# Performance work log

Hardware: AMD Instinct MI355X
Metric: run time of the kernel (lower is better)

## Reference

```python
import jax, jax.numpy as jnp
import numpy as np
from jax import lax

S, V, E, H, T = 2048, 50257, 512, 1024, 12
HD = H // 2  # per-direction hidden
START, END = 0, 1
NEG = -1e6


def setup_inputs() -> dict:
    key = jax.random.key(0)
    ks = jax.random.split(key, 16)
    sentence = jax.random.randint(ks[0], (S,), 0, V)
    gold_tags = jax.random.randint(ks[1], (S,), 2, T)  # avoid START/END gold labels
    emb = jax.random.normal(ks[2], (V, E), jnp.float32) * 0.1
    s = 0.05
    wih_f = jax.random.normal(ks[3], (4 * HD, E), jnp.float32) * s
    whh_f = jax.random.normal(ks[4], (4 * HD, HD), jnp.float32) * s
    b_f = jax.random.normal(ks[5], (4 * HD,), jnp.float32) * s
    wih_b = jax.random.normal(ks[6], (4 * HD, E), jnp.float32) * s
    whh_b = jax.random.normal(ks[7], (4 * HD, HD), jnp.float32) * s
    b_b = jax.random.normal(ks[8], (4 * HD,), jnp.float32) * s
    w_out = jax.random.normal(ks[9], (T, H), jnp.float32) * s
    b_out = jax.random.normal(ks[10], (T,), jnp.float32) * s
    transitions = jax.random.normal(ks[11], (T, T), jnp.float32)
    transitions = transitions.at[START, :].set(NEG).at[:, END].set(NEG)
    h0 = jax.random.normal(ks[12], (2, HD), jnp.float32)
    c0 = jax.random.normal(ks[13], (2, HD), jnp.float32)
    return dict(sentence=sentence, gold_tags=gold_tags, emb=emb,
                wih_f=wih_f, whh_f=whh_f, b_f=b_f,
                wih_b=wih_b, whh_b=whh_b, b_b=b_b,
                w_out=w_out, b_out=b_out, transitions=transitions,
                h0=h0, c0=c0)


def _lstm_dir(x, h0, c0, wih, whh, b):
    # x: [S, E] -> hidden states [S, HD]; PyTorch gate order i,f,g,o
    def step(carry, xt):
        h, c = carry
        g = xt @ wih.T + h @ whh.T + b
        i, f, gg, o = jnp.split(g, 4)
        i, f, o = jax.nn.sigmoid(i), jax.nn.sigmoid(f), jax.nn.sigmoid(o)
        c = f * c + i * jnp.tanh(gg)
        h = o * jnp.tanh(c)
        return (h, c), h
    _, hs = lax.scan(step, (h0, c0), x)
    return hs


def _feats(sentence, emb, wih_f, whh_f, b_f, wih_b, whh_b, b_b, w_out, b_out, h0, c0):
    x = emb[sentence]                                  # [S, E]
    hf = _lstm_dir(x, h0[0], c0[0], wih_f, whh_f, b_f)  # [S, HD]
    hb = _lstm_dir(x[::-1], h0[1], c0[1], wih_b, whh_b, b_b)[::-1]
    return jnp.concatenate([hf, hb], axis=1) @ w_out.T + b_out  # [S, T]


def _crf_nll(feats, gold_tags, transitions):
    # forward algorithm (log partition)
    init = jnp.full((T,), NEG, feats.dtype).at[START].set(0.0)
    def step(prev, feat):
        nxt = jax.nn.logsumexp(prev[None, :] + transitions + feat[:, None], axis=1)
        return nxt, None
    final, _ = lax.scan(step, init, feats)
    alpha = jax.nn.logsumexp(final + transitions[END])
    # gold score
    tags = jnp.concatenate([jnp.array([START], gold_tags.dtype), gold_tags])
    trans_score = jnp.sum(transitions[tags[1:], tags[:-1]])
    emit_score = jnp.sum(feats[jnp.arange(feats.shape[0]), tags[1:]])
    gold = trans_score + emit_score + transitions[END, tags[-1]]
    return alpha - gold


def reference(sentence, gold_tags, emb, wih_f, whh_f, b_f, wih_b, whh_b, b_b,
              w_out, b_out, transitions, h0, c0):
    feats = _feats(sentence, emb, wih_f, whh_f, b_f, wih_b, whh_b, b_b,
                   w_out, b_out, h0, c0)
    return _crf_nll(feats, gold_tags, transitions)
```

## Files before the change

### kernel.cpp

```cpp
#include <hip/hip_runtime.h>
#include <hip/hip_bf16.h>

#define S 2048
#define HD 512
#define EDIM 512
#define NT 12
#define G4 2048
#define NWGD 64
#define RPW 32
#define JPW 8
#define HSTR 36

typedef unsigned short ushort_t;
typedef unsigned int uint_t;

__device__ __forceinline__ ushort_t f2b(float f) {
    uint_t u = __float_as_uint(f);
    uint_t r = u + 0x7fffu + ((u >> 16) & 1u);
    return (ushort_t)(r >> 16);
}
__device__ __forceinline__ float b2f(ushort_t h) {
    return __uint_as_float(((uint_t)h) << 16);
}
__device__ __forceinline__ float sigm(float x) { return 1.f / (1.f + __expf(-x)); }
__device__ __forceinline__ float tanh_(float x) {
    float e = __expf(2.f * x);
    return 1.f - 2.f / (e + 1.f);
}

__global__ __launch_bounds__(256, 2)
void xw_gemm(const int* __restrict__ sentence, const float* __restrict__ emb,
             const float* __restrict__ wih_f, const float* __restrict__ b_f,
             const float* __restrict__ wih_b, const float* __restrict__ b_b,
             ushort_t* __restrict__ xw) {
    __shared__ float As[32][68];
    __shared__ float Bs[32][68];
    __shared__ int toks[64];
    const int tid = threadIdx.x;
    const int tbase = blockIdx.x * 64;
    const int rbase = blockIdx.y * 64;
    const int dir = blockIdx.z;
    const float* wih = dir ? wih_b : wih_f;
    const float* bia = dir ? b_b : b_f;
    if (tid < 64) {
        int tt = tbase + tid;
        toks[tid] = sentence[dir ? (S - 1 - tt) : tt];
    }
    __syncthreads();
    const int lm = tid >> 2;
    const int lk = (tid & 3) * 8;
    const int ty = tid >> 4, tx = tid & 15;
    const float* aBase = emb + (size_t)toks[lm] * EDIM + lk;
    const float* bBase = wih + (size_t)(rbase + lm) * EDIM + lk;
    float acc[4][4];
#pragma unroll
    for (int i = 0; i < 4; ++i)
#pragma unroll
        for (int j = 0; j < 4; ++j) acc[i][j] = 0.f;

    for (int kc = 0; kc < EDIM; kc += 32) {
        float4 a0 = ((const float4*)(aBase + kc))[0];
        float4 a1 = ((const float4*)(aBase + kc))[1];
        float4 b0 = ((const float4*)(bBase + kc))[0];
        float4 b1 = ((const float4*)(bBase + kc))[1];
        __syncthreads();
        As[lk + 0][lm] = a0.x; As[lk + 1][lm] = a0.y; As[lk + 2][lm] = a0.z; As[lk + 3][lm] = a0.w;
        As[lk + 4][lm] = a1.x; As[lk + 5][lm] = a1.y; As[lk + 6][lm] = a1.z; As[lk + 7][lm] = a1.w;
        Bs[lk + 0][lm] = b0.x; Bs[lk + 1][lm] = b0.y; Bs[lk + 2][lm] = b0.z; Bs[lk + 3][lm] = b0.w;
        Bs[lk + 4][lm] = b1.x; Bs[lk + 5][lm] = b1.y; Bs[lk + 6][lm] = b1.z; Bs[lk + 7][lm] = b1.w;
        __syncthreads();
#pragma unroll
        for (int kk = 0; kk < 32; ++kk) {
            float4 a4 = *(const float4*)&As[kk][ty * 4];
            float4 b4 = *(const float4*)&Bs[kk][tx * 4];
            float av[4] = {a4.x, a4.y, a4.z, a4.w};
            float bv[4] = {b4.x, b4.y, b4.z, b4.w};
#pragma unroll
            for (int i = 0; i < 4; ++i)
#pragma unroll
                for (int j = 0; j < 4; ++j) acc[i][j] = fmaf(av[i], bv[j], acc[i][j]);
        }
    }
    float4 bi = *(const float4*)&bia[rbase + tx * 4];
    float bvv[4] = {bi.x, bi.y, bi.z, bi.w};
#pragma unroll
    for (int i = 0; i < 4; ++i) {
        ushort4 o;
        o.x = f2b(acc[i][0] + bvv[0]);
        o.y = f2b(acc[i][1] + bvv[1]);
        o.z = f2b(acc[i][2] + bvv[2]);
        o.w = f2b(acc[i][3] + bvv[3]);
        ushort_t* p = xw + ((size_t)dir * S + tbase + ty * 4 + i) * G4 + rbase + tx * 4;
        *(ushort4*)p = o;
    }
}

__global__ __launch_bounds__(256, 1)
void lstm_rec(const float* __restrict__ whh_f, const float* __restrict__ whh_b,
              const float* __restrict__ h0, const float* __restrict__ c0,
              const ushort_t* __restrict__ xw, float* hs) {
    __shared__ float hstage[16 * HSTR];
    __shared__ float gates[RPW];
    const int tid = threadIdx.x;
    const int dir = blockIdx.x >> 6;
    const int wg = blockIdx.x & 63;
    const int jbase = wg * JPW;
    const int rg = tid >> 4, kc = tid & 15;
    const float* whh = dir ? whh_b : whh_f;

    int grow[2];
#pragma unroll
    for (int ri = 0; ri < 2; ++ri) {
        int r = rg * 2 + ri;
        grow[ri] = (r >> 3) * HD + jbase + (r & 7);
    }
    float4 w[2][8];
#pragma unroll
    for (int ri = 0; ri < 2; ++ri)
#pragma unroll
        for (int i = 0; i < 8; ++i)
            w[ri][i] = *(const float4*)&whh[(size_t)grow[ri] * HD + kc * 32 + i * 4];

    const ushort_t* xwd = xw + (size_t)dir * S * G4;
    float* hsd = hs + (size_t)dir * S * HD;

    float cj = 0.f;
    if (tid < JPW) cj = c0[dir * HD + jbase + tid];

    {
        int c = tid >> 4, m = (2 * tid) & 31;
        hstage[c * HSTR + m] = h0[dir * HD + 2 * tid];
        hstage[c * HSTR + m + 1] = h0[dir * HD + 2 * tid + 1];
    }
    __syncthreads();

    const bool isw = (kc == 0);
    for (int t = 0; t < S; ++t) {
        float xv0 = 0.f, xv1 = 0.f;
        if (isw) {
            xv0 = b2f(xwd[(size_t)t * G4 + grow[0]]);
            xv1 = b2f(xwd[(size_t)t * G4 + grow[1]]);
        }
        float a0 = 0.f, a1 = 0.f;
#pragma unroll
        for (int i = 0; i < 8; ++i) {
            float4 h4 = *(const float4*)&hstage[kc * HSTR + i * 4];
            a0 = fmaf(w[0][i].x, h4.x, a0); a0 = fmaf(w[0][i].y, h4.y, a0);
            a0 = fmaf(w[0][i].z, h4.z, a0); a0 = fmaf(w[0][i].w, h4.w, a0);
            a1 = fmaf(w[1][i].x, h4.x, a1); a1 = fmaf(w[1][i].y, h4.y, a1);
            a1 = fmaf(w[1][i].z, h4.z, a1); a1 = fmaf(w[1][i].w, h4.w, a1);
        }
#pragma unroll
        for (int m = 1; m < 16; m <<= 1) {
            a0 += __shfl_xor(a0, m);
            a1 += __shfl_xor(a1, m);
        }
        if (isw) {
            gates[rg * 2] = a0 + xv0;
            gates[rg * 2 + 1] = a1 + xv1;
        }
        __syncthreads();
        if (tid < JPW) {
            float ai = gates[tid], af = gates[JPW + tid];
            float ag = gates[2 * JPW + tid], ao = gates[3 * JPW + tid];
            float ii = sigm(ai), ff = sigm(af), gg = tanh_(ag), oo = sigm(ao);
            cj = ff * cj + ii * gg;
            float hnew = oo * tanh_(cj);
            __hip_atomic_store(&hsd[(size_t)t * HD + jbase + tid], hnew,
                               __ATOMIC_RELAXED, __HIP_MEMORY_SCOPE_AGENT);
        }
        if (t < S - 1) {
            const unsigned long long* p0 =
                (const unsigned long long*)&hsd[(size_t)t * HD + 2 * tid];
            float v0, v1;
            for (;;) {
                unsigned long long v =
                    __hip_atomic_load(p0, __ATOMIC_RELAXED, __HIP_MEMORY_SCOPE_AGENT);
                uint_t lo = (uint_t)v, hi = (uint_t)(v >> 32);
                if (lo != 0xFFFFFFFFu && hi != 0xFFFFFFFFu) {
                    v0 = __uint_as_float(lo);
                    v1 = __uint_as_float(hi);
                    break;
                }
            }
            int c = tid >> 4, m = (2 * tid) & 31;
            hstage[c * HSTR + m] = v0;
            hstage[c * HSTR + m + 1] = v1;
        }
        __syncthreads();
    }
}

__global__ __launch_bounds__(256)
void feats_k(const float* __restrict__ hs, const float* __restrict__ w_out,
             const float* __restrict__ b_out, float* __restrict__ feats) {
    const int t = blockIdx.x, tid = threadIdx.x;
    float4 h4;
    if (tid < 128)
        h4 = *(const float4*)&hs[(size_t)t * HD + tid * 4];
    else
        h4 = *(const float4*)&hs[(size_t)S * HD + (size_t)(S - 1 - t) * HD + (tid - 128) * 4];
    float acc[NT];
#pragma unroll
    for (int tg = 0; tg < NT; ++tg) {
        float4 w4 = *(const float4*)&w_out[(size_t)tg * 1024 + tid * 4];
        acc[tg] = h4.x * w4.x + h4.y * w4.y + h4.z * w4.z + h4.w * w4.w;
    }
#pragma unroll
    for (int m = 1; m < 64; m <<= 1)
#pragma unroll
        for (int tg = 0; tg < NT; ++tg) acc[tg] += __shfl_xor(acc[tg], m);
    __shared__ float part[4][NT];
    if ((tid & 63) == 0) {
#pragma unroll
        for (int tg = 0; tg < NT; ++tg) part[tid >> 6][tg] = acc[tg];
    }
    __syncthreads();
    if (tid < NT)
        feats[(size_t)t * NT + tid] =
            part[0][tid] + part[1][tid] + part[2][tid] + part[3][tid] + b_out[tid];
}

__global__ __launch_bounds__(256, 1)
void crf_k(const float* __restrict__ feats, const int* __restrict__ gold,
           const float* __restrict__ trans, float* __restrict__ out) {
    extern __shared__ float sfeats[];
    __shared__ float red[256];
    __shared__ float nprev[NT];
    __shared__ float tr[144];
    __shared__ float gold_sh;
    const int tid = threadIdx.x;
    for (int i = tid; i < S * NT / 4; i += 256)
        ((float4*)sfeats)[i] = ((const float4*)feats)[i];
    if (tid < 144) tr[tid] = trans[tid];
    __syncthreads();
    float gsum = 0.f;
    for (int t = tid; t < S; t += 256) {
        int a = gold[t];
        int b = t ? gold[t - 1] : 0;
        gsum += tr[a * NT + b] + sfeats[t * NT + a];
    }
    red[tid] = gsum;
    __syncthreads();
    for (int s = 128; s; s >>= 1) {
        if (tid < s) red[tid] += red[tid + s];
        __syncthreads();
    }
    if (tid == 0) gold_sh = red[0] + tr[1 * NT + gold[S - 1]];
    __syncthreads();
    const int i = tid >> 4, j = tid & 15;
    const bool act = (tid < 192) && (j < NT);
    float tij = act ? tr[i * NT + j] : -3e38f;
    float prev = (j == 0) ? 0.f : -1e6f;
    for (int t = 0; t < S; ++t) {
        float v = act ? (prev + tij) : -3e38f;
        float mx = v;
        mx = fmaxf(mx, __shfl_xor(mx, 1));
        mx = fmaxf(mx, __shfl_xor(mx, 2));
        mx = fmaxf(mx, __shfl_xor(mx, 4));
        mx = fmaxf(mx, __shfl_xor(mx, 8));
        float e = __expf(v - mx);
        float ss = e;
        ss += __shfl_xor(ss, 1);
        ss += __shfl_xor(ss, 2);
        ss += __shfl_xor(ss, 4);
        ss += __shfl_xor(ss, 8);
        if (tid < 192 && j == 0) nprev[i] = mx + __logf(ss) + sfeats[t * NT + i];
        __syncthreads();
        prev = nprev[j < NT ? j : 0];
        __syncthreads();
    }
    if (tid < 64) {
        float v2 = (tid < NT) ? prev + tr[1 * NT + tid] : -3e38f;
        float mx = v2;
        mx = fmaxf(mx, __shfl_xor(mx, 1));
        mx = fmaxf(mx, __shfl_xor(mx, 2));
        mx = fmaxf(mx, __shfl_xor(mx, 4));
        mx = fmaxf(mx, __shfl_xor(mx, 8));
        float e = __expf(v2 - mx);
        float ss = e;
        ss += __shfl_xor(ss, 1);
        ss += __shfl_xor(ss, 2);
        ss += __shfl_xor(ss, 4);
        ss += __shfl_xor(ss, 8);
        if (tid == 0) out[0] = (mx + __logf(ss)) - gold_sh;
    }
}

extern "C" void kernel_launch(void* const* d_in, const int* in_sizes, int n_in,
                              void* d_out, int out_size, void* d_ws, size_t ws_size,
                              hipStream_t stream) {
    const int* sentence = (const int*)d_in[0];
    const int* gold = (const int*)d_in[1];
    const float* emb = (const float*)d_in[2];
    const float* wih_f = (const float*)d_in[3];
    const float* whh_f = (const float*)d_in[4];
    const float* b_f = (const float*)d_in[5];
    const float* wih_b = (const float*)d_in[6];
    const float* whh_b = (const float*)d_in[7];
    const float* b_b = (const float*)d_in[8];
    const float* w_out = (const float*)d_in[9];
    const float* b_out = (const float*)d_in[10];
    const float* trans = (const float*)d_in[11];
    const float* h0 = (const float*)d_in[12];
    const float* c0 = (const float*)d_in[13];
    float* out = (float*)d_out;

    char* ws = (char*)d_ws;
    const size_t XW_B = (size_t)2 * S * G4 * 2;
    const size_t HS_B = (size_t)2 * S * HD * 4;
    ushort_t* xw = (ushort_t*)ws;
    float* hs = (float*)(ws + XW_B);
    float* feats = (float*)(ws + XW_B + HS_B);

    hipMemsetAsync(hs, 0xFF, HS_B, stream);

    dim3 gg(S / 64, G4 / 64, 2);
    xw_gemm<<<gg, 256, 0, stream>>>(sentence, emb, wih_f, b_f, wih_b, b_b, xw);

    lstm_rec<<<2 * NWGD, 256, 0, stream>>>(whh_f, whh_b, h0, c0, xw, hs);

    feats_k<<<S, 256, 0, stream>>>(hs, w_out, b_out, feats);

    const size_t CRF_LDS = (size_t)S * NT * 4;
    hipFuncSetAttribute((const void*)crf_k,
                        hipFuncAttributeMaxDynamicSharedMemorySize, (int)CRF_LDS);
    crf_k<<<1, 256, CRF_LDS, stream>>>(feats, gold, trans, out);
}
```

Before: 5.393 ms.

## Make LSTM recurrence wave-independent with per-wave h copies and staged transposed xw

The input projection output is written transposed (gate-row major, time contiguous) so each wave can prefetch 64 timesteps of its gate inputs into LDS in a double buffer. Within the recurrent kernel, each wave now owns two hidden units: it computes all four gate dot products using 8 lanes per row, reduces with shuffles, and keeps a private copy of the full hidden state in LDS. This removes both __syncthreads per timestep and the shared gates buffer. Each wave polls global memory for the full previous h vector, which raises global polling traffic per step, and correctness now depends on per-wave program order.

Measured after the change: 8.596 ms. 1.59x slower.

```diff
diff --git a/kernel.cpp b/kernel.cpp
--- a/kernel.cpp
+++ b/kernel.cpp
@@ -7,9 +7,7 @@
 #define NT 12
 #define G4 2048
 #define NWGD 64
-#define RPW 32
 #define JPW 8
-#define HSTR 36
 
 typedef unsigned short ushort_t;
 typedef unsigned int uint_t;
@@ -32,7 +30,7 @@
 void xw_gemm(const int* __restrict__ sentence, const float* __restrict__ emb,
              const float* __restrict__ wih_f, const float* __restrict__ b_f,
              const float* __restrict__ wih_b, const float* __restrict__ b_b,
-             ushort_t* __restrict__ xw) {
+             ushort_t* __restrict__ xwT) {
     __shared__ float As[32][68];
     __shared__ float Bs[32][68];
     __shared__ int toks[64];
@@ -58,11 +56,11 @@
 #pragma unroll
         for (int j = 0; j < 4; ++j) acc[i][j] = 0.f;
 
-    for (int kc = 0; kc < EDIM; kc += 32) {
-        float4 a0 = ((const float4*)(aBase + kc))[0];
-        float4 a1 = ((const float4*)(aBase + kc))[1];
-        float4 b0 = ((const float4*)(bBase + kc))[0];
-        float4 b1 = ((const float4*)(bBase + kc))[1];
+    for (int kcc = 0; kcc < EDIM; kcc += 32) {
+        float4 a0 = ((const float4*)(aBase + kcc))[0];
+        float4 a1 = ((const float4*)(aBase + kcc))[1];
+        float4 b0 = ((const float4*)(bBase + kcc))[0];
+        float4 b1 = ((const float4*)(bBase + kcc))[1];
         __syncthreads();
         As[lk + 0][lm] = a0.x; As[lk + 1][lm] = a0.y; As[lk + 2][lm] = a0.z; As[lk + 3][lm] = a0.w;
         As[lk + 4][lm] = a1.x; As[lk + 5][lm] = a1.y; As[lk + 6][lm] = a1.z; As[lk + 7][lm] = a1.w;
@@ -84,13 +82,13 @@
     float4 bi = *(const float4*)&bia[rbase + tx * 4];
     float bvv[4] = {bi.x, bi.y, bi.z, bi.w};
 #pragma unroll
-    for (int i = 0; i < 4; ++i) {
+    for (int j = 0; j < 4; ++j) {
         ushort4 o;
-        o.x = f2b(acc[i][0] + bvv[0]);
-        o.y = f2b(acc[i][1] + bvv[1]);
-        o.z = f2b(acc[i][2] + bvv[2]);
-        o.w = f2b(acc[i][3] + bvv[3]);
-        ushort_t* p = xw + ((size_t)dir * S + tbase + ty * 4 + i) * G4 + rbase + tx * 4;
+        o.x = f2b(acc[0][j] + bvv[j]);
+        o.y = f2b(acc[1][j] + bvv[j]);
+        o.z = f2b(acc[2][j] + bvv[j]);
+        o.w = f2b(acc[3][j] + bvv[j]);
+        ushort_t* p = xwT + ((size_t)dir * G4 + rbase + tx * 4 + j) * S + tbase + ty * 4;
         *(ushort4*)p = o;
     }
 }
@@ -98,96 +96,106 @@
 __global__ __launch_bounds__(256, 1)
 void lstm_rec(const float* __restrict__ whh_f, const float* __restrict__ whh_b,
               const float* __restrict__ h0, const float* __restrict__ c0,
-              const ushort_t* __restrict__ xw, float* hs) {
-    __shared__ float hstage[16 * HSTR];
-    __shared__ float gates[RPW];
+              const ushort_t* __restrict__ xwT, float* hs) {
+    __shared__ float hstage[4 * 544];
+    __shared__ ushort_t xstage[4][2][512];
     const int tid = threadIdx.x;
+    const int wv = tid >> 6;
+    const int lw = tid & 63;
     const int dir = blockIdx.x >> 6;
     const int wg = blockIdx.x & 63;
     const int jbase = wg * JPW;
-    const int rg = tid >> 4, kc = tid & 15;
+    const int kc = lw & 7;
+    const int gate = (lw >> 3) & 3;
+    const int jl = lw >> 5;
+    const int jglob = jbase + wv * 2 + jl;
+    const int row = gate * HD + jglob;
     const float* whh = dir ? whh_b : whh_f;
 
-    int grow[2];
-#pragma unroll
-    for (int ri = 0; ri < 2; ++ri) {
-        int r = rg * 2 + ri;
-        grow[ri] = (r >> 3) * HD + jbase + (r & 7);
-    }
-    float4 w[2][8];
-#pragma unroll
-    for (int ri = 0; ri < 2; ++ri)
-#pragma unroll
-        for (int i = 0; i < 8; ++i)
-            w[ri][i] = *(const float4*)&whh[(size_t)grow[ri] * HD + kc * 32 + i * 4];
-
-    const ushort_t* xwd = xw + (size_t)dir * S * G4;
+    float4 w[16];
+#pragma unroll
+    for (int i = 0; i < 16; ++i)
+        w[i] = *(const float4*)&whh[(size_t)row * HD + kc * 64 + i * 4];
+
+    const ushort_t* xwd = xwT + (size_t)dir * G4 * S;
     float* hsd = hs + (size_t)dir * S * HD;
 
-    float cj = 0.f;
-    if (tid < JPW) cj = c0[dir * HD + jbase + tid];
-
+    const int ri = lw >> 3;
+    const ushort_t* sbase = xwd + (size_t)((ri >> 1) * HD + jbase + wv * 2 + (ri & 1)) * S;
     {
-        int c = tid >> 4, m = (2 * tid) & 31;
-        hstage[c * HSTR + m] = h0[dir * HD + 2 * tid];
-        hstage[c * HSTR + m + 1] = h0[dir * HD + 2 * tid + 1];
-    }
-    __syncthreads();
-
-    const bool isw = (kc == 0);
+        uint4 vch = *(const uint4*)(sbase + (lw & 7) * 8);
+        *(uint4*)&xstage[wv][0][ri * 64 + (lw & 7) * 8] = vch;
+    }
+
+    const bool upd = (lw & 31) == 0;
+    float cj = upd ? c0[dir * HD + jglob] : 0.f;
+
+    {
+        float4 a = *(const float4*)&h0[dir * HD + lw * 8];
+        float4 b4 = *(const float4*)&h0[dir * HD + lw * 8 + 4];
+        float* d = &hstage[wv * 544 + (lw >> 3) * 68 + (lw & 7) * 8];
+        *(float4*)d = a;
+        *(float4*)(d + 4) = b4;
+    }
+
+    const float* hb = &hstage[wv * 544 + kc * 68];
     for (int t = 0; t < S; ++t) {
-        float xv0 = 0.f, xv1 = 0.f;
-        if (isw) {
-            xv0 = b2f(xwd[(size_t)t * G4 + grow[0]]);
-            xv1 = b2f(xwd[(size_t)t * G4 + grow[1]]);
-        }
-        float a0 = 0.f, a1 = 0.f;
-#pragma unroll
-        for (int i = 0; i < 8; ++i) {
-            float4 h4 = *(const float4*)&hstage[kc * HSTR + i * 4];
-            a0 = fmaf(w[0][i].x, h4.x, a0); a0 = fmaf(w[0][i].y, h4.y, a0);
-            a0 = fmaf(w[0][i].z, h4.z, a0); a0 = fmaf(w[0][i].w, h4.w, a0);
-            a1 = fmaf(w[1][i].x, h4.x, a1); a1 = fmaf(w[1][i].y, h4.y, a1);
-            a1 = fmaf(w[1][i].z, h4.z, a1); a1 = fmaf(w[1][i].w, h4.w, a1);
-        }
-#pragma unroll
-        for (int m = 1; m < 16; m <<= 1) {
-            a0 += __shfl_xor(a0, m);
-            a1 += __shfl_xor(a1, m);
-        }
-        if (isw) {
-            gates[rg * 2] = a0 + xv0;
-            gates[rg * 2 + 1] = a1 + xv1;
-        }
-        __syncthreads();
-        if (tid < JPW) {
-            float ai = gates[tid], af = gates[JPW + tid];
-            float ag = gates[2 * JPW + tid], ao = gates[3 * JPW + tid];
-            float ii = sigm(ai), ff = sigm(af), gg = tanh_(ag), oo = sigm(ao);
-            cj = ff * cj + ii * gg;
+        if ((t & 63) == 0 && t + 64 < S) {
+            uint4 vch = *(const uint4*)(sbase + (t + 64) + (lw & 7) * 8);
+            *(uint4*)&xstage[wv][((t >> 6) + 1) & 1][ri * 64 + (lw & 7) * 8] = vch;
+        }
+        float4 a4 = {0.f, 0.f, 0.f, 0.f};
+#pragma unroll
+        for (int i = 0; i < 16; ++i) {
+            float4 h4 = *(const float4*)&hb[i * 4];
+            a4.x = fmaf(w[i].x, h4.x, a4.x);
+            a4.y = fmaf(w[i].y, h4.y, a4.y);
+            a4.z = fmaf(w[i].z, h4.z, a4.z);
+            a4.w = fmaf(w[i].w, h4.w, a4.w);
+        }
+        float acc = (a4.x + a4.y) + (a4.z + a4.w);
+        acc += __shfl_xor(acc, 1);
+        acc += __shfl_xor(acc, 2);
+        acc += __shfl_xor(acc, 4);
+        const int gb = lw & 32;
+        float g0 = __shfl(acc, gb);
+        float g1 = __shfl(acc, gb + 8);
+        float g2 = __shfl(acc, gb + 16);
+        float g3 = __shfl(acc, gb + 24);
+        if (upd) {
+            const ushort_t* xs = &xstage[wv][(t >> 6) & 1][jl * 64 + (t & 63)];
+            float gi = g0 + b2f(xs[0]);
+            float gf = g1 + b2f(xs[128]);
+            float gg = g2 + b2f(xs[256]);
+            float go = g3 + b2f(xs[384]);
+            float ii = sigm(gi), ff = sigm(gf), gv = tanh_(gg), oo = sigm(go);
+            cj = ff * cj + ii * gv;
             float hnew = oo * tanh_(cj);
-            __hip_atomic_store(&hsd[(size_t)t * HD + jbase + tid], hnew,
+            __hip_atomic_store(&hsd[(size_t)t * HD + jglob], hnew,
                                __ATOMIC_RELAXED, __HIP_MEMORY_SCOPE_AGENT);
         }
         if (t < S - 1) {
-            const unsigned long long* p0 =
-                (const unsigned long long*)&hsd[(size_t)t * HD + 2 * tid];
-            float v0, v1;
-            for (;;) {
-                unsigned long long v =
-                    __hip_atomic_load(p0, __ATOMIC_RELAXED, __HIP_MEMORY_SCOPE_AGENT);
-                uint_t lo = (uint_t)v, hi = (uint_t)(v >> 32);
-                if (lo != 0xFFFFFFFFu && hi != 0xFFFFFFFFu) {
-                    v0 = __uint_as_float(lo);
-                    v1 = __uint_as_float(hi);
-                    break;
-                }
+            const unsigned long long* pb = (const unsigned long long*)&hsd[(size_t)t * HD];
+            unsigned long long v[4];
+            unsigned msk = 0;
+            do {
+#pragma unroll
+                for (int q = 0; q < 4; ++q)
+                    if (!(msk & (1u << q))) {
+                        unsigned long long x = __hip_atomic_load(
+                            pb + lw + 64 * q, __ATOMIC_RELAXED, __HIP_MEMORY_SCOPE_AGENT);
+                        if ((uint_t)x != 0xFFFFFFFFu && (uint_t)(x >> 32) != 0xFFFFFFFFu) {
+                            v[q] = x;
+                            msk |= 1u << q;
+                        }
+                    }
+            } while (msk != 15u);
+#pragma unroll
+            for (int q = 0; q < 4; ++q) {
+                int p = 2 * lw + 128 * q;
+                *(unsigned long long*)&hstage[wv * 544 + (p >> 6) * 68 + (p & 63)] = v[q];
             }
-            int c = tid >> 4, m = (2 * tid) & 31;
-            hstage[c * HSTR + m] = v0;
-            hstage[c * HSTR + m + 1] = v1;
-        }
-        __syncthreads();
+        }
     }
 }
 
@@ -309,16 +317,16 @@
     char* ws = (char*)d_ws;
     const size_t XW_B = (size_t)2 * S * G4 * 2;
     const size_t HS_B = (size_t)2 * S * HD * 4;
-    ushort_t* xw = (ushort_t*)ws;
+    ushort_t* xwT = (ushort_t*)ws;
     float* hs = (float*)(ws + XW_B);
     float* feats = (float*)(ws + XW_B + HS_B);
 
     hipMemsetAsync(hs, 0xFF, HS_B, stream);
 
     dim3 gg(S / 64, G4 / 64, 2);
-    xw_gemm<<<gg, 256, 0, stream>>>(sentence, emb, wih_f, b_f, wih_b, b_b, xw);
-
-    lstm_rec<<<2 * NWGD, 256, 0, stream>>>(whh_f, whh_b, h0, c0, xw, hs);
+    xw_gemm<<<gg, 256, 0, stream>>>(sentence, emb, wih_f, b_f, wih_b, b_b, xwT);
+
+    lstm_rec<<<2 * NWGD, 256, 0, stream>>>(whh_f, whh_b, h0, c0, xwT, hs);
 
     feats_k<<<S, 256, 0, stream>>>(hs, w_out, b_out, feats);
 
```
